# Kernel tuning notes

Measured on AMD Instinct MI355X. Metric: run time of the kernel, lower is better.

The kernel has to match this reference:

```python
import jax, jax.numpy as jnp
import numpy as np

LEVELS = 16
FEATURES = 2
HASHMAP_SIZE = 524288  # 2**19
BASE_RES = 16
PER_LEVEL_SCALE = 1.5
N_POINTS = 2097152  # 2**21

# Per-level grid resolutions, computed exactly like the torch code: int(base*scale**l)
_RES = np.array([int(BASE_RES * PER_LEVEL_SCALE ** l) for l in range(LEVELS)], dtype=np.float32)

# Instant-NGP spatial hash primes
_P1, _P2, _P3 = np.int32(73856093), np.int32(19349663), np.int32(83492791)


def setup_inputs() -> dict:
    key = jax.random.key(0)
    k1, k2 = jax.random.split(key)
    x = jax.random.uniform(k1, (N_POINTS, 3), dtype=jnp.float32)
    # Stacked learned hash tables: [L, T, F], init randn*0.01 as in the module
    tables = jax.random.normal(k2, (LEVELS, HASHMAP_SIZE, FEATURES), dtype=jnp.float32) * 0.01
    return {"x": x, "tables": tables}


def reference(x, tables):
    # x: [N, 3] float; tables: [L, T, F] float
    res = jnp.asarray(_RES)                       # [L]
    pos = x[None, :, :] * res[:, None, None]      # [L, N, 3]
    p = jnp.floor(pos).astype(jnp.int32)          # [L, N, 3] (matches torch .int())
    # Spatial hash with int32 wrap-around, identical to torch int32 semantics
    h = (p[..., 0] * _P1) ^ (p[..., 1] * _P2) ^ (p[..., 2] * _P3)
    idx = jnp.mod(h, np.int32(HASHMAP_SIZE))      # [L, N], nonnegative (sign of divisor)
    emb = jax.vmap(lambda t, i: t[i])(tables, idx)  # [L, N, F] per-level gather
    n = x.shape[0]
    # concat over levels along last dim -> [N, L*F]
    return jnp.transpose(emb, (1, 0, 2)).reshape(n, LEVELS * FEATURES)
```

## Files before the change

### kernel.cpp

```cpp
#include <hip/hip_runtime.h>

#define LEVELS 16
#define TSIZE 524288
#define TMASK (TSIZE - 1)
#define TPB 256
#define GPPT 8
#define CHUNK (TPB * GPPT)

typedef float f2v __attribute__((ext_vector_type(2)));
typedef float f4v __attribute__((ext_vector_type(4)));

__device__ __constant__ float c_res[LEVELS] = {
    16.f, 24.f, 36.f, 54.f, 81.f, 121.f, 182.f, 273.f,
    410.f, 615.f, 922.f, 1383.f, 2075.f, 3113.f, 4670.f, 7006.f
};

__device__ __forceinline__ unsigned hash_idx(float px, float py, float pz, float r)
{
    const int ix = (int)floorf(px * r);
    const int iy = (int)floorf(py * r);
    const int iz = (int)floorf(pz * r);
    const unsigned h = (unsigned)ix * 73856093u
                     ^ (unsigned)iy * 19349663u
                     ^ (unsigned)iz * 83492791u;
    return h & TMASK;
}


__global__ __launch_bounds__(TPB) void gather_kernel(
    const float* __restrict__ x,
    const float* __restrict__ tables,
    f2v* __restrict__ ws,
    int n, int bpl)
{
    __shared__ float xs[CHUNK * 3];
    const int b = blockIdx.x;
    const int half = b / (8 * bpl);
    const int r = b % (8 * bpl);
    const int level = half * 8 + (r & 7);
    const int c = r >> 3;
    const int t = threadIdx.x;

    const float rs = c_res[level];
    const float* __restrict__ tbl = tables + (size_t)level * (TSIZE * 2);
    f2v* __restrict__ slab = ws + ((size_t)c * LEVELS + level) * CHUNK;
    const long long base = (long long)c * CHUNK;

    if (base + CHUNK <= n) {
        const f4v* __restrict__ xg = reinterpret_cast<const f4v*>(x + 3 * base);
#pragma unroll
        for (int j = 0; j < 6; ++j) {
            const int s = j * TPB + t;
            *reinterpret_cast<f4v*>(&xs[4 * s]) = xg[s];
        }
        __syncthreads();

        unsigned idx[GPPT];
#pragma unroll
        for (int j = 0; j < GPPT; ++j) {
            const int local = j * TPB + t;
            const float px = xs[3 * local + 0];
            const float py = xs[3 * local + 1];
            const float pz = xs[3 * local + 2];
            idx[j] = hash_idx(px, py, pz, rs);
        }

        f2v e[GPPT];
#pragma unroll
        for (int j = 0; j < GPPT; ++j)
            e[j] = *reinterpret_cast<const f2v*>(tbl + 2 * (size_t)idx[j]);

#pragma unroll
        for (int j = 0; j < GPPT; ++j)
            __builtin_nontemporal_store(e[j], slab + j * TPB + t);
    } else {
#pragma unroll
        for (int j = 0; j < GPPT; ++j) {
            const int local = j * TPB + t;
            const long long p = base + local;
            if (p < n) {
                const float qx = x[3 * p + 0];
                const float qy = x[3 * p + 1];
                const float qz = x[3 * p + 2];
                const unsigned idx = hash_idx(qx, qy, qz, rs);
                const f2v e = *reinterpret_cast<const f2v*>(tbl + 2 * (size_t)idx);
                __builtin_nontemporal_store(e, slab + local);
            }
        }
    }
}

__global__ __launch_bounds__(TPB) void assemble_kernel(
    const f2v* __restrict__ ws,
    float* __restrict__ out,
    int n)
{
    const int c = blockIdx.x;
    const int t = threadIdx.x;
    const int q = t & 7;
    const int sub = t >> 3;

    const f2v* __restrict__ wa = ws + ((size_t)c * LEVELS + 2 * q) * CHUNK;
    const f2v* __restrict__ wb = wa + CHUNK;
    const long long base = (long long)c * CHUNK;

    if (base + CHUNK <= n) {
#pragma unroll 8
        for (int u = 0; u < CHUNK / 64; ++u) {
            const int lp = 2 * (u * 32 + sub);
            const f4v a = __builtin_nontemporal_load(
                reinterpret_cast<const f4v*>(wa + lp));
            const f4v b = __builtin_nontemporal_load(
                reinterpret_cast<const f4v*>(wb + lp));
            f4v v0, v1;
            v0.x = a.x; v0.y = a.y; v0.z = b.x; v0.w = b.y;
            v1.x = a.z; v1.y = a.w; v1.z = b.z; v1.w = b.w;
            float* row = out + (size_t)(base + lp) * (2 * LEVELS) + 4 * q;
            __builtin_nontemporal_store(v0, reinterpret_cast<f4v*>(row));
            __builtin_nontemporal_store(v1, reinterpret_cast<f4v*>(row + 2 * LEVELS));
        }
    } else {
#pragma unroll 8
        for (int u = 0; u < CHUNK / 32; ++u) {
            const int lp = u * 32 + sub;
            const long long pt = base + lp;
            if (pt < n) {
                const f2v a = __builtin_nontemporal_load(wa + lp);
                const f2v b = __builtin_nontemporal_load(wb + lp);
                f4v v;
                v.x = a.x; v.y = a.y; v.z = b.x; v.w = b.y;
                __builtin_nontemporal_store(
                    v, reinterpret_cast<f4v*>(out + (size_t)pt * (2 * LEVELS) + 4 * q));
            }
        }
    }
}

#define ROWW 34
__global__ __launch_bounds__(TPB) void hashgrid_fused(
    const float* __restrict__ x,
    const float* __restrict__ tables,
    float* __restrict__ out,
    int n)
{
    __shared__ float lds[TPB * ROWW];
    const int t = threadIdx.x;

    for (long long base = (long long)blockIdx.x * TPB; base < n;
         base += (long long)gridDim.x * TPB) {
        const int p = (int)base + t;
        float px = 0.f, py = 0.f, pz = 0.f;
        if (p < n) {
            px = x[3 * (size_t)p + 0];
            py = x[3 * (size_t)p + 1];
            pz = x[3 * (size_t)p + 2];
        }
#pragma unroll
        for (int l = 0; l < LEVELS; ++l) {
            if (p < n) {
                const unsigned idx = hash_idx(px, py, pz, c_res[l]);
                const f2v e = *reinterpret_cast<const f2v*>(
                    tables + (((size_t)l * TSIZE + idx) << 1));
                *reinterpret_cast<f2v*>(lds + t * ROWW + 2 * l) = e;
            }
            __syncthreads();
        }
#pragma unroll
        for (int it = 0; it < 8; ++it) {
            const int lp = it * 32 + (t >> 3);
            const int qq = t & 7;
            const int gp = (int)base + lp;
            if (gp < n) {
                const f2v a = *reinterpret_cast<const f2v*>(lds + lp * ROWW + 4 * qq);
                const f2v b = *reinterpret_cast<const f2v*>(lds + lp * ROWW + 4 * qq + 2);
                f4v v;
                v.x = a.x; v.y = a.y; v.z = b.x; v.w = b.y;
                __builtin_nontemporal_store(
                    v, reinterpret_cast<f4v*>(out + (size_t)gp * (2 * LEVELS) + 4 * qq));
            }
        }
        __syncthreads();
    }
}

extern "C" void kernel_launch(void* const* d_in, const int* in_sizes, int n_in,
                              void* d_out, int out_size, void* d_ws, size_t ws_size,
                              hipStream_t stream)
{
    const float* x      = (const float*)d_in[0];
    const float* tables = (const float*)d_in[1];
    float* out          = (float*)d_out;
    const int n = in_sizes[0] / 3;

    const int bpl = (n + CHUNK - 1) / CHUNK;
    const size_t ws_need = (size_t)bpl * LEVELS * CHUNK * sizeof(f2v);
    if (ws_size < ws_need) {
        int grid = 1024;
        const int nblocks = (n + TPB - 1) / TPB;
        if (nblocks < grid) grid = nblocks;
        hashgrid_fused<<<grid, TPB, 0, stream>>>(x, tables, out, n);
        return;
    }

    f2v* ws = (f2v*)d_ws;
    gather_kernel<<<2 * 8 * bpl, TPB, 0, stream>>>(x, tables, ws, n, bpl);
    assemble_kernel<<<bpl, TPB, 0, stream>>>(ws, out, n);
}
```

Baseline: 339.6 us.

## Precompute all level hash indices in a separate kernel before gathering

Adds a hash_kernel that reads each point once and writes all 16 per-level hash indices to a workspace buffer. gather_kernel then reads these precomputed indices instead of reloading and rehashing x for every level. This is meant to remove the repeated per-level reads of x and the hash arithmetic from the gather pass. In exchange it adds a 4-byte-per-level index write and read, plus an extra kernel launch. When the workspace is too small for the index buffer, a fallback gather_x_kernel loads x straight into registers instead of staging it through shared memory.

```diff
diff --git a/kernel.cpp b/kernel.cpp
--- a/kernel.cpp
+++ b/kernel.cpp
@@ -27,13 +27,60 @@
 }
 
 
+
+__global__ __launch_bounds__(TPB) void hash_kernel(
+    const float* __restrict__ x,
+    unsigned* __restrict__ idxw,
+    int n)
+{
+    __shared__ float xs[CHUNK * 3];
+    const int c = blockIdx.x;
+    const int t = threadIdx.x;
+    const long long base = (long long)c * CHUNK;
+    unsigned* __restrict__ islab = idxw + (size_t)c * LEVELS * CHUNK;
+
+    if (base + CHUNK <= n) {
+        const f4v* __restrict__ xg = reinterpret_cast<const f4v*>(x + 3 * base);
+#pragma unroll
+        for (int j = 0; j < 6; ++j) {
+            const int s = j * TPB + t;
+            *reinterpret_cast<f4v*>(&xs[4 * s]) = xg[s];
+        }
+        __syncthreads();
+
+#pragma unroll
+        for (int j = 0; j < GPPT; ++j) {
+            const int local = j * TPB + t;
+            const float px = xs[3 * local + 0];
+            const float py = xs[3 * local + 1];
+            const float pz = xs[3 * local + 2];
+#pragma unroll
+            for (int l = 0; l < LEVELS; ++l) {
+                const unsigned id = hash_idx(px, py, pz, c_res[l]);
+                __builtin_nontemporal_store(id, islab + l * CHUNK + local);
+            }
+        }
+    } else {
+        for (int j = 0; j < GPPT; ++j) {
+            const int local = j * TPB + t;
+            const long long p = base + local;
+            if (p < n) {
+                const float px = x[3 * p + 0];
+                const float py = x[3 * p + 1];
+                const float pz = x[3 * p + 2];
+                for (int l = 0; l < LEVELS; ++l)
+                    islab[l * CHUNK + local] = hash_idx(px, py, pz, c_res[l]);
+            }
+        }
+    }
+}
+
 __global__ __launch_bounds__(TPB) void gather_kernel(
-    const float* __restrict__ x,
+    const unsigned* __restrict__ idxr,
     const float* __restrict__ tables,
     f2v* __restrict__ ws,
     int n, int bpl)
 {
-    __shared__ float xs[CHUNK * 3];
     const int b = blockIdx.x;
     const int half = b / (8 * bpl);
     const int r = b % (8 * bpl);
@@ -41,35 +88,73 @@
     const int c = r >> 3;
     const int t = threadIdx.x;
 
+    const float* __restrict__ tbl = tables + (size_t)level * (TSIZE * 2);
+    f2v* __restrict__ slab = ws + ((size_t)c * LEVELS + level) * CHUNK;
+    const unsigned* __restrict__ islab = idxr + ((size_t)c * LEVELS + level) * CHUNK;
+    const long long base = (long long)c * CHUNK;
+
+    if (base + CHUNK <= n) {
+        unsigned idx[GPPT];
+#pragma unroll
+        for (int j = 0; j < GPPT; ++j)
+            idx[j] = islab[j * TPB + t];
+
+        f2v e[GPPT];
+#pragma unroll
+        for (int j = 0; j < GPPT; ++j)
+            e[j] = *reinterpret_cast<const f2v*>(tbl + 2 * (size_t)idx[j]);
+
+#pragma unroll
+        for (int j = 0; j < GPPT; ++j)
+            __builtin_nontemporal_store(e[j], slab + j * TPB + t);
+    } else {
+        for (int j = 0; j < GPPT; ++j) {
+            const int local = j * TPB + t;
+            if (base + local < n) {
+                const unsigned id = islab[local];
+                const f2v e = *reinterpret_cast<const f2v*>(tbl + 2 * (size_t)id);
+                __builtin_nontemporal_store(e, slab + local);
+            }
+        }
+    }
+}
+
+__global__ __launch_bounds__(TPB) void gather_x_kernel(
+    const float* __restrict__ x,
+    const float* __restrict__ tables,
+    f2v* __restrict__ ws,
+    int n, int bpl)
+{
+    const int b = blockIdx.x;
+    const int half = b / (8 * bpl);
+    const int r = b % (8 * bpl);
+    const int level = half * 8 + (r & 7);
+    const int c = r >> 3;
+    const int t = threadIdx.x;
+
     const float rs = c_res[level];
     const float* __restrict__ tbl = tables + (size_t)level * (TSIZE * 2);
     f2v* __restrict__ slab = ws + ((size_t)c * LEVELS + level) * CHUNK;
     const long long base = (long long)c * CHUNK;
 
     if (base + CHUNK <= n) {
-        const f4v* __restrict__ xg = reinterpret_cast<const f4v*>(x + 3 * base);
-#pragma unroll
-        for (int j = 0; j < 6; ++j) {
-            const int s = j * TPB + t;
-            *reinterpret_cast<f4v*>(&xs[4 * s]) = xg[s];
-        }
-        __syncthreads();
-
+        const float* __restrict__ xb = x + 3 * base;
+        float px[GPPT], py[GPPT], pz[GPPT];
+#pragma unroll
+        for (int j = 0; j < GPPT; ++j) {
+            const int local = j * TPB + t;
+            px[j] = xb[3 * local + 0];
+            py[j] = xb[3 * local + 1];
+            pz[j] = xb[3 * local + 2];
+        }
         unsigned idx[GPPT];
 #pragma unroll
-        for (int j = 0; j < GPPT; ++j) {
-            const int local = j * TPB + t;
-            const float px = xs[3 * local + 0];
-            const float py = xs[3 * local + 1];
-            const float pz = xs[3 * local + 2];
-            idx[j] = hash_idx(px, py, pz, rs);
-        }
-
+        for (int j = 0; j < GPPT; ++j)
+            idx[j] = hash_idx(px[j], py[j], pz[j], rs);
         f2v e[GPPT];
 #pragma unroll
         for (int j = 0; j < GPPT; ++j)
             e[j] = *reinterpret_cast<const f2v*>(tbl + 2 * (size_t)idx[j]);
-
 #pragma unroll
         for (int j = 0; j < GPPT; ++j)
             __builtin_nontemporal_store(e[j], slab + j * TPB + t);
@@ -193,8 +278,10 @@
     const int n = in_sizes[0] / 3;
 
     const int bpl = (n + CHUNK - 1) / CHUNK;
-    const size_t ws_need = (size_t)bpl * LEVELS * CHUNK * sizeof(f2v);
-    if (ws_size < ws_need) {
+    const size_t slab_bytes = (size_t)bpl * LEVELS * CHUNK * sizeof(f2v);
+    const size_t idx_bytes  = (size_t)bpl * LEVELS * CHUNK * sizeof(unsigned);
+
+    if (ws_size < slab_bytes) {
         int grid = 1024;
         const int nblocks = (n + TPB - 1) / TPB;
         if (nblocks < grid) grid = nblocks;
@@ -203,6 +290,13 @@
     }
 
     f2v* ws = (f2v*)d_ws;
-    gather_kernel<<<2 * 8 * bpl, TPB, 0, stream>>>(x, tables, ws, n, bpl);
+
+    if (ws_size >= slab_bytes + idx_bytes) {
+        unsigned* idxw = (unsigned*)((char*)d_ws + slab_bytes);
+        hash_kernel<<<bpl, TPB, 0, stream>>>(x, idxw, n);
+        gather_kernel<<<2 * 8 * bpl, TPB, 0, stream>>>(idxw, tables, ws, n, bpl);
+    } else {
+        gather_x_kernel<<<2 * 8 * bpl, TPB, 0, stream>>>(x, tables, ws, n, bpl);
+    }
     assemble_kernel<<<bpl, TPB, 0, stream>>>(ws, out, n);
 }
```

Result: slower. 351.4 us (+3.5%).
